# Performance work log

Measured on AMD Instinct MI355X. Metric: run time of the kernel, lower is better.

## Reference

```python
import jax, jax.numpy as jnp
import numpy as np

N = 100000   # nodes
D = 64       # in_features
E = 1200000  # edges (avg degree ~12)
C = 1.0      # curvature
MIN_NORM = 1e-15
PROJ_EPS = 4e-3  # float32 eps used by HGCN-style PoincareBall.proj


def setup_inputs() -> dict:
    key = jax.random.key(0)
    k1, k2, k3 = jax.random.split(key, 3)
    x = jax.random.normal(k1, (N, D), dtype=jnp.float32) * 0.1
    edge_index = jax.random.randint(k2, (2, E), 0, N, dtype=jnp.int32)
    # GCNConv learned params (lin weight + bias)
    W = jax.random.normal(k3, (D, D), dtype=jnp.float32) / np.sqrt(D)
    b = jnp.zeros((D,), dtype=jnp.float32)
    return {"x": x, "W": W, "b": b, "edge_index": edge_index}


def expmap0(u, c):
    sqrt_c = jnp.sqrt(c)
    u_norm = jnp.maximum(jnp.linalg.norm(u, axis=-1, keepdims=True), MIN_NORM)
    return jnp.tanh(sqrt_c * u_norm) * u / (sqrt_c * u_norm)


def proj(x, c):
    norm = jnp.maximum(jnp.linalg.norm(x, axis=-1, keepdims=True), MIN_NORM)
    maxnorm = (1.0 - PROJ_EPS) / jnp.sqrt(c)
    return jnp.where(norm > maxnorm, x / norm * maxnorm, x)


def gcn_conv(x, W, b, edge_index, n_nodes):
    # PyG GCNConv: h = x @ W; add self-loops; symmetric normalization; scatter-add; + bias
    h = x @ W  # [N, D]
    src, dst = edge_index[0], edge_index[1]
    loops = jnp.arange(n_nodes, dtype=edge_index.dtype)
    s = jnp.concatenate([src, loops])  # [E+N]
    d = jnp.concatenate([dst, loops])
    deg = jax.ops.segment_sum(jnp.ones(s.shape, dtype=h.dtype), d, num_segments=n_nodes)
    deg_inv_sqrt = jnp.where(deg > 0, deg ** -0.5, 0.0)
    norm = deg_inv_sqrt[s] * deg_inv_sqrt[d]  # [E+N]
    msgs = h[s] * norm[:, None]               # gather + scale: [E+N, D]
    out = jax.ops.segment_sum(msgs, d, num_segments=n_nodes)  # scatter-add
    return out + b


def reference(x, W, b, edge_index):
    # Note: original computes logmap0(x) but discards it (conv uses raw x) -- dead code.
    support_t = gcn_conv(x, W, b, edge_index, N)
    return proj(expmap0(support_t, C), C)
```

## Files before the change

kernel.cpp:

```cpp
#include <hip/hip_runtime.h>
#include <hip/hip_bf16.h>

#define DFEAT 64
#define NBSH  8
#define NPB   256
#define EPB   4096
#define EPT   (EPB / 256)
#define CAPB  3584
#define REGS  4608
#define BSTR  32

__global__ __launch_bounds__(256) void part_kernel(const int* __restrict__ ei,
                                                   int* __restrict__ bcnt,
                                                   unsigned* __restrict__ ebuf, int E) {
    __shared__ int h[512];
    __shared__ int base[512];
    int t = threadIdx.x;
    h[t] = 0; h[t + 256] = 0;
    __syncthreads();
    int bb = blockIdx.x * EPB;
    int sv[EPT], dv[EPT];
    #pragma unroll
    for (int i = 0; i < EPT; ++i) {
        int e = bb + i * 256 + t;
        if (e < E) {
            sv[i] = ei[e];
            dv[i] = ei[E + e];
            atomicAdd(&h[dv[i] >> NBSH], 1);
        } else dv[i] = -1;
    }
    __syncthreads();
    base[t]       = h[t]       ? atomicAdd(&bcnt[t * BSTR],         h[t])       : 0;
    base[t + 256] = h[t + 256] ? atomicAdd(&bcnt[(t + 256) * BSTR], h[t + 256]) : 0;
    __syncthreads();
    h[t] = 0; h[t + 256] = 0;
    __syncthreads();
    #pragma unroll
    for (int i = 0; i < EPT; ++i) {
        if (dv[i] >= 0) {
            int bkt = dv[i] >> NBSH;
            int pos = base[bkt] + atomicAdd(&h[bkt], 1);
            if (pos < CAPB)
                ebuf[(size_t)bkt * REGS + pos] =
                    (unsigned)sv[i] | ((unsigned)(dv[i] & (NPB - 1)) << 17);
        }
    }
}

__global__ __launch_bounds__(256) void csr_kernel(const int* __restrict__ bcnt,
                                                  unsigned* __restrict__ buf,
                                                  int* __restrict__ begs,
                                                  int* __restrict__ lens,
                                                  float* __restrict__ dinv, int n) {
    __shared__ unsigned eb[CAPB];
    __shared__ int cnt[256];
    __shared__ int tmp[256];
    int t = threadIdx.x, b = blockIdx.x;
    int ecnt = bcnt[b * BSTR]; if (ecnt > CAPB) ecnt = CAPB;
    size_t rb = (size_t)b * REGS;

    const uint4* bufv = (const uint4*)(buf + rb);
    uint4* ebv = (uint4*)eb;
    int nv = (ecnt + 3) >> 2;
    for (int i = t; i < nv; i += 256) ebv[i] = bufv[i];
    cnt[t] = 0;
    __syncthreads();
    for (int i = t; i < ecnt; i += 256) atomicAdd(&cnt[eb[i] >> 17], 1);
    __syncthreads();

    int nid = (b << NBSH) + t;
    int deg = cnt[t];
    int slots = (nid < n) ? ((deg + 4) & ~3) : 0;
    tmp[t] = slots;
    __syncthreads();
    int s = slots;
    for (int o = 1; o < 256; o <<= 1) {
        int y = (t >= o) ? tmp[t - o] : 0;
        __syncthreads();
        tmp[t] += y;
        __syncthreads();
    }
    int excl = tmp[t] - s;
    int beg = (int)rb + excl;
    if (nid < n) {
        begs[nid] = beg;
        lens[nid] = slots;
        dinv[nid] = rsqrtf((float)(deg + 1));
        buf[beg] = (unsigned)nid;
        for (int k = deg + 1; k < slots; ++k) buf[beg + k] = (unsigned)n;
    }
    cnt[t] = excl + 1;
    __syncthreads();
    for (int i = t; i < ecnt; i += 256) {
        unsigned v = eb[i];
        int pos = atomicAdd(&cnt[v >> 17], 1);
        buf[rb + pos] = v & 0x1ffffu;
    }
}

__global__ __launch_bounds__(256) void xsprep_kernel(const float* __restrict__ x,
                                                     const float* __restrict__ dinv,
                                                     unsigned* __restrict__ xs, int n) {
    int i = blockIdx.x * blockDim.x + threadIdx.x;
    int total = (n + 1) * 32;
    if (i >= total) return;
    int row = i >> 5, col = i & 31;
    unsigned v = 0;
    if (row < n) {
        float di = dinv[row];
        float f0 = x[(size_t)row * DFEAT + 2 * col] * di;
        float f1 = x[(size_t)row * DFEAT + 2 * col + 1] * di;
        unsigned u0 = __float_as_uint(f0); u0 = (u0 + 0x7fffu + ((u0 >> 16) & 1u)) >> 16;
        unsigned u1 = __float_as_uint(f1); u1 = (u1 + 0x7fffu + ((u1 >> 16) & 1u)) >> 16;
        v = (u0 & 0xffffu) | (u1 << 16);
    }
    xs[i] = v;
}

__global__ __launch_bounds__(256) void agg_kernel(const int* __restrict__ begs,
                                                  const int* __restrict__ lens,
                                                  const int* __restrict__ srcs,
                                                  const float* __restrict__ dinv,
                                                  const uint2* __restrict__ xs2,
                                                  const float* __restrict__ W,
                                                  const float* __restrict__ b,
                                                  float* __restrict__ out,
                                                  int n, int noctets) {
    __shared__ float Wl[DFEAT * DFEAT];
    __shared__ float xl[8][DFEAT];
    int t = threadIdx.x;
    #pragma unroll
    for (int i = 0; i < 16; ++i) Wl[i * 256 + t] = W[i * 256 + t];
    __syncthreads();

    int r = t >> 6, lane = t & 63;
    int g = lane >> 4;
    int q = lane & 15;
    float bias = b[lane];

    for (int oct = blockIdx.x; oct < noctets; oct += gridDim.x) {
        int na = oct * 8 + r;
        int nb_ = na + 4;
        bool va = na < n, vb = nb_ < n;
        if (!va) continue;

        int beg0 = begs[na],  end0 = beg0 + lens[na];
        int beg1 = 0, end1 = 0;
        if (vb) { beg1 = begs[nb_]; end1 = beg1 + lens[nb_]; }

        float a0 = 0, a1 = 0, a2 = 0, a3 = 0;
        float b0 = 0, b1 = 0, b2 = 0, b3 = 0;
        int base0 = beg0, base1 = beg1;
        while (base0 < end0 || base1 < end1) {
            int m0 = end0 - base0; m0 = m0 < 0 ? 0 : (m0 > 64 ? 64 : m0);
            int m1 = end1 - base1; m1 = m1 < 0 ? 0 : (m1 > 64 ? 64 : m1);
            int idx0 = 0, idx1 = 0;
            if (lane < m0) idx0 = srcs[base0 + lane];
            if (lane < m1) idx1 = srcs[base1 + lane];
            int q0 = m0 >> 2, q1 = m1 >> 2;
            int qc = q0 < q1 ? q0 : q1;
            #pragma unroll 4
            for (int j = 0; j < qc; ++j) {
                int sv0 = __shfl(idx0, 4 * j + g, 64);
                int sv1 = __shfl(idx1, 4 * j + g, 64);
                uint2 d0 = xs2[(unsigned)sv0 * 16 + q];
                uint2 d1 = xs2[(unsigned)sv1 * 16 + q];
                a0 += __uint_as_float(d0.x << 16);
                a1 += __uint_as_float(d0.x & 0xffff0000u);
                a2 += __uint_as_float(d0.y << 16);
                a3 += __uint_as_float(d0.y & 0xffff0000u);
                b0 += __uint_as_float(d1.x << 16);
                b1 += __uint_as_float(d1.x & 0xffff0000u);
                b2 += __uint_as_float(d1.y << 16);
                b3 += __uint_as_float(d1.y & 0xffff0000u);
            }
            #pragma unroll 4
            for (int j = qc; j < q0; ++j) {
                int sv0 = __shfl(idx0, 4 * j + g, 64);
                uint2 d0 = xs2[(unsigned)sv0 * 16 + q];
                a0 += __uint_as_float(d0.x << 16);
                a1 += __uint_as_float(d0.x & 0xffff0000u);
                a2 += __uint_as_float(d0.y << 16);
                a3 += __uint_as_float(d0.y & 0xffff0000u);
            }
            #pragma unroll 4
            for (int j = qc; j < q1; ++j) {
                int sv1 = __shfl(idx1, 4 * j + g, 64);
                uint2 d1 = xs2[(unsigned)sv1 * 16 + q];
                b0 += __uint_as_float(d1.x << 16);
                b1 += __uint_as_float(d1.x & 0xffff0000u);
                b2 += __uint_as_float(d1.y << 16);
                b3 += __uint_as_float(d1.y & 0xffff0000u);
            }
            base0 += 64; base1 += 64;
        }
        #pragma unroll
        for (int off = 16; off < 64; off <<= 1) {
            a0 += __shfl_xor(a0, off, 64);
            a1 += __shfl_xor(a1, off, 64);
            a2 += __shfl_xor(a2, off, 64);
            a3 += __shfl_xor(a3, off, 64);
            b0 += __shfl_xor(b0, off, 64);
            b1 += __shfl_xor(b1, off, 64);
            b2 += __shfl_xor(b2, off, 64);
            b3 += __shfl_xor(b3, off, 64);
        }
        if (g == 0) {
            float dia = dinv[na];
            xl[r][4 * q + 0] = a0 * dia;
            xl[r][4 * q + 1] = a1 * dia;
            xl[r][4 * q + 2] = a2 * dia;
            xl[r][4 * q + 3] = a3 * dia;
            if (vb) {
                float dib = dinv[nb_];
                xl[r + 4][4 * q + 0] = b0 * dib;
                xl[r + 4][4 * q + 1] = b1 * dib;
                xl[r + 4][4 * q + 2] = b2 * dib;
                xl[r + 4][4 * q + 3] = b3 * dib;
            }
        }

        float oa0 = bias, oa1 = 0.0f, ob0 = bias, ob1 = 0.0f;
        #pragma unroll
        for (int k = 0; k < DFEAT; k += 2) {
            float w0 = Wl[k * DFEAT + lane];
            float w1 = Wl[(k + 1) * DFEAT + lane];
            oa0 = fmaf(xl[r][k],     w0, oa0);
            oa1 = fmaf(xl[r][k + 1], w1, oa1);
            ob0 = fmaf(xl[r + 4][k],     w0, ob0);
            ob1 = fmaf(xl[r + 4][k + 1], w1, ob1);
        }
        float oa = oa0 + oa1;
        float ob = ob0 + ob1;

        float ssa = oa * oa, ssb = ob * ob;
        #pragma unroll
        for (int off = 32; off > 0; off >>= 1) {
            ssa += __shfl_xor(ssa, off, 64);
            ssb += __shfl_xor(ssb, off, 64);
        }
        float norma = fmaxf(sqrtf(ssa), 1e-15f);
        float sca = fminf(tanhf(norma), 1.0f - 4e-3f) / norma;
        out[(long long)na * DFEAT + lane] = oa * sca;
        if (vb) {
            float normb = fmaxf(sqrtf(ssb), 1e-15f);
            float scb = fminf(tanhf(normb), 1.0f - 4e-3f) / normb;
            out[(long long)nb_ * DFEAT + lane] = ob * scb;
        }
    }
}


extern "C" void kernel_launch(void* const* d_in, const int* in_sizes, int n_in,
                              void* d_out, int out_size, void* d_ws, size_t ws_size,
                              hipStream_t stream) {
    const float* x = (const float*)d_in[0];
    const float* W = (const float*)d_in[1];
    const float* b = (const float*)d_in[2];
    const int* ei  = (const int*)d_in[3];

    int n = in_sizes[0] / DFEAT;
    int E = in_sizes[3] / 2;
    int NBUCK = (n + NPB - 1) / NPB;
    int nblk = (E + EPB - 1) / EPB;
    int noctets = (n + 7) / 8;

    int* bcnt = (int*)d_ws;
    unsigned* buf = (unsigned*)(bcnt + 512 * BSTR);
    int* begs = (int*)(buf + (size_t)NBUCK * REGS);
    int* lens = begs + n;
    float* dinv = (float*)(lens + n);
    size_t xsoff = (size_t)(((int*)dinv + n) - (int*)d_ws);
    xsoff = (xsoff + 31) & ~(size_t)31;
    unsigned* xs = (unsigned*)d_ws + xsoff;

    float* out = (float*)d_out;

    int aggblocks = 2048;
    if (aggblocks > noctets) aggblocks = noctets;
    int xsblocks = ((n + 1) * 32 + 255) / 256;

    hipMemsetAsync(bcnt, 0, 512 * BSTR * sizeof(int), stream);
    part_kernel  <<<nblk, 256, 0, stream>>>(ei, bcnt, buf, E);
    csr_kernel   <<<NBUCK, 256, 0, stream>>>(bcnt, buf, begs, lens, dinv, n);
    xsprep_kernel<<<xsblocks, 256, 0, stream>>>(x, dinv, xs, n);
    agg_kernel   <<<aggblocks, 256, 0, stream>>>(begs, lens, (const int*)buf, dinv,
                                                 (const uint2*)xs, W, b, out, n, noctets);
}
```

Baseline: 180.7 us.

## Pack row begin/length into int2 and split aggregation into four launches

Row begin and slot count are now stored together as one int2 array, so the aggregation kernel does a single 8-byte load per node instead of two separate 4-byte loads from different arrays. The aggregation work is also split into four sequential launches, each covering a quarter of the node octets with up to 2048 blocks. The split appears intended to improve cache locality of gathered features or load balance per launch. It adds three extra kernel launches plus the W-to-shared-memory reload in each launch.

```diff
diff --git a/kernel.cpp b/kernel.cpp
--- a/kernel.cpp
+++ b/kernel.cpp
@@ -49,8 +49,7 @@
 
 __global__ __launch_bounds__(256) void csr_kernel(const int* __restrict__ bcnt,
                                                   unsigned* __restrict__ buf,
-                                                  int* __restrict__ begs,
-                                                  int* __restrict__ lens,
+                                                  int2* __restrict__ bl,
                                                   float* __restrict__ dinv, int n) {
     __shared__ unsigned eb[CAPB];
     __shared__ int cnt[256];
@@ -83,8 +82,7 @@
     int excl = tmp[t] - s;
     int beg = (int)rb + excl;
     if (nid < n) {
-        begs[nid] = beg;
-        lens[nid] = slots;
+        bl[nid] = make_int2(beg, slots);
         dinv[nid] = rsqrtf((float)(deg + 1));
         buf[beg] = (unsigned)nid;
         for (int k = deg + 1; k < slots; ++k) buf[beg + k] = (unsigned)n;
@@ -117,15 +115,14 @@
     xs[i] = v;
 }
 
-__global__ __launch_bounds__(256) void agg_kernel(const int* __restrict__ begs,
-                                                  const int* __restrict__ lens,
+__global__ __launch_bounds__(256) void agg_kernel(const int2* __restrict__ bl,
                                                   const int* __restrict__ srcs,
                                                   const float* __restrict__ dinv,
                                                   const uint2* __restrict__ xs2,
                                                   const float* __restrict__ W,
                                                   const float* __restrict__ b,
                                                   float* __restrict__ out,
-                                                  int n, int noctets) {
+                                                  int n, int octbase, int octend) {
     __shared__ float Wl[DFEAT * DFEAT];
     __shared__ float xl[8][DFEAT];
     int t = threadIdx.x;
@@ -138,15 +135,16 @@
     int q = lane & 15;
     float bias = b[lane];
 
-    for (int oct = blockIdx.x; oct < noctets; oct += gridDim.x) {
+    for (int oct = octbase + blockIdx.x; oct < octend; oct += gridDim.x) {
         int na = oct * 8 + r;
         int nb_ = na + 4;
         bool va = na < n, vb = nb_ < n;
         if (!va) continue;
 
-        int beg0 = begs[na],  end0 = beg0 + lens[na];
+        int2 p0 = bl[na];
+        int beg0 = p0.x, end0 = p0.x + p0.y;
         int beg1 = 0, end1 = 0;
-        if (vb) { beg1 = begs[nb_]; end1 = beg1 + lens[nb_]; }
+        if (vb) { int2 p1 = bl[nb_]; beg1 = p1.x; end1 = p1.x + p1.y; }
 
         float a0 = 0, a1 = 0, a2 = 0, a3 = 0;
         float b0 = 0, b1 = 0, b2 = 0, b3 = 0;
@@ -267,23 +265,28 @@
 
     int* bcnt = (int*)d_ws;
     unsigned* buf = (unsigned*)(bcnt + 512 * BSTR);
-    int* begs = (int*)(buf + (size_t)NBUCK * REGS);
-    int* lens = begs + n;
-    float* dinv = (float*)(lens + n);
+    int2* bl = (int2*)(buf + (size_t)NBUCK * REGS);
+    float* dinv = (float*)(bl + n);
     size_t xsoff = (size_t)(((int*)dinv + n) - (int*)d_ws);
     xsoff = (xsoff + 31) & ~(size_t)31;
     unsigned* xs = (unsigned*)d_ws + xsoff;
 
     float* out = (float*)d_out;
 
-    int aggblocks = 2048;
-    if (aggblocks > noctets) aggblocks = noctets;
     int xsblocks = ((n + 1) * 32 + 255) / 256;
 
     hipMemsetAsync(bcnt, 0, 512 * BSTR * sizeof(int), stream);
     part_kernel  <<<nblk, 256, 0, stream>>>(ei, bcnt, buf, E);
-    csr_kernel   <<<NBUCK, 256, 0, stream>>>(bcnt, buf, begs, lens, dinv, n);
+    csr_kernel   <<<NBUCK, 256, 0, stream>>>(bcnt, buf, bl, dinv, n);
     xsprep_kernel<<<xsblocks, 256, 0, stream>>>(x, dinv, xs, n);
-    agg_kernel   <<<aggblocks, 256, 0, stream>>>(begs, lens, (const int*)buf, dinv,
-                                                 (const uint2*)xs, W, b, out, n, noctets);
-}
+
+    int Q = (noctets + 3) / 4;
+    for (int qd = 0; qd < 4; ++qd) {
+        int ob = qd * Q;
+        int oe = ob + Q; if (oe > noctets) oe = noctets;
+        if (ob >= oe) break;
+        int blks = oe - ob; if (blks > 2048) blks = 2048;
+        agg_kernel<<<blks, 256, 0, stream>>>(bl, (const int*)buf, dinv,
+                                             (const uint2*)xs, W, b, out, n, ob, oe);
+    }
+}
```

After: 192.1 us. 1.06x slower.
